# Performance work log

Hardware: AMD Instinct MI355X
Metric: run time of the kernel (lower is better)

Reference implementation:

```python
import jax, jax.numpy as jnp
import numpy as np

C = 0.1          # curvature
EPS = 1e-8
BN_EPS = 1e-5
MAX_NORM = 0.9

def batchnorm_train(x, gamma, beta):
    mu = jnp.mean(x, axis=0)
    var = jnp.var(x, axis=0)  # biased, matches torch BN normalization
    return gamma * (x - mu) * jax.lax.rsqrt(var + BN_EPS) + beta

def euclidean_to_poincare(x, c=C, max_norm=MAX_NORM):
    norm = jnp.linalg.norm(x, axis=-1, keepdims=True)
    zeros_mask = norm == 0
    safe_norm = jnp.where(zeros_mask, jnp.ones_like(norm), norm)
    sqrt_c = jnp.sqrt(jnp.asarray(c, x.dtype))
    scale = max_norm * jnp.tanh(sqrt_c * norm) / (sqrt_c * safe_norm)
    return jnp.where(zeros_mask, jnp.zeros_like(x), scale * x)

def poincare_to_euclidean(x, c=C):
    norms = jnp.linalg.norm(x, axis=-1, keepdims=True)
    norms = jnp.clip(norms, 1e-8, 1.0 - 1e-8)
    sqrt_c = jnp.sqrt(jnp.asarray(c, x.dtype))
    return x * jnp.arctanh(sqrt_c * norms) / (sqrt_c * norms)

def batch_poincare_exp_map(x, v, c=C):
    x_nsq = jnp.sum(x * x, axis=-1, keepdims=True)
    lambda_x = 2.0 / (1.0 - c * x_nsq + EPS)
    v_norm = jnp.linalg.norm(v, axis=-1, keepdims=True)
    v_norm = jnp.maximum(v_norm, EPS)
    sqrt_c = jnp.sqrt(jnp.asarray(c, x.dtype))
    scale = jnp.tanh(sqrt_c * lambda_x * v_norm / 2.0) / (sqrt_c * v_norm)
    sv = scale * v
    numerator = (1.0 - c * x_nsq) * sv
    x_sv = jnp.sum(x * sv, axis=-1, keepdims=True)
    sv_nsq = jnp.sum(sv * sv, axis=-1, keepdims=True)
    denom = 1.0 - 2.0 * c * x_sv + c * c * x_nsq * sv_nsq
    result = x + numerator / (denom + EPS)
    mask = jnp.all(jnp.isfinite(result), axis=-1, keepdims=True)
    return jnp.where(mask, result, jnp.zeros_like(result))

def batch_poincare_log_map(x, y, c=C):
    x_nsq = jnp.sum(x * x, axis=-1, keepdims=True)
    lambda_x = 2.0 / (1.0 - c * x_nsq + EPS)
    y_nsq = jnp.sum(y * y, axis=-1, keepdims=True)
    xy = jnp.sum(x * y, axis=-1, keepdims=True)
    numerator = (1.0 - 2.0 * c * xy + c * y_nsq) * x - (1.0 - c * x_nsq) * y
    denom = 1.0 - 2.0 * c * xy + c * c * x_nsq * y_nsq
    diff = numerator / (denom + EPS)
    diff_norm = jnp.linalg.norm(diff, axis=-1, keepdims=True)
    diff_norm = jnp.maximum(diff_norm, EPS)
    sqrt_c = jnp.sqrt(jnp.asarray(c, x.dtype))
    return 2.0 / (sqrt_c * lambda_x) * jnp.arctanh(sqrt_c * diff_norm) * diff / diff_norm

def setup_inputs() -> dict:
    key = jax.random.key(0)
    ks = jax.random.split(key, 8)
    B, D_IN, H, D_OUT = 8192, 1024, 2048, 1000
    x = jax.random.normal(ks[0], (B, D_IN), dtype=jnp.float32)
    # kaiming_normal fan_out: std = sqrt(2/fan_out) with fan_out = out_features
    W1 = jax.random.normal(ks[1], (H, D_IN), dtype=jnp.float32) * np.sqrt(2.0 / H)
    b1 = jnp.zeros((H,), jnp.float32)
    g1 = jnp.ones((H,), jnp.float32)
    be1 = jnp.zeros((H,), jnp.float32)
    W2 = jax.random.normal(ks[2], (H, H), dtype=jnp.float32) * np.sqrt(2.0 / H)
    b2 = jnp.zeros((H,), jnp.float32)
    g2 = jnp.ones((H,), jnp.float32)
    be2 = jnp.zeros((H,), jnp.float32)
    W3 = jax.random.normal(ks[3], (D_OUT, H), dtype=jnp.float32) * np.sqrt(2.0 / D_OUT)
    b3 = jnp.zeros((D_OUT,), jnp.float32)
    return {"x": x, "W1": W1, "b1": b1, "g1": g1, "be1": be1,
            "W2": W2, "b2": b2, "g2": g2, "be2": be2, "W3": W3, "b3": b3}

def reference(x, W1, b1, g1, be1, W2, b2, g2, be2, W3, b3):
    h1 = jax.nn.relu(batchnorm_train(x @ W1.T + b1, g1, be1))
    h1_hyp = euclidean_to_poincare(h1)
    origin = jnp.zeros_like(h1_hyp)
    h1_tan = batch_poincare_log_map(origin, h1_hyp)
    h2_tan = jax.nn.relu(batchnorm_train(h1_tan @ W2.T + b2, g2, be2))
    h2_hyp = batch_poincare_exp_map(origin, h2_tan)
    h2_euc = poincare_to_euclidean(h2_hyp)
    out = h2_euc @ W3.T + b3
    return jax.nn.log_softmax(out, axis=1)
```

## Files before the change

kernel.cpp:

```cpp
#include <hip/hip_runtime.h>

typedef __bf16 bf16x8 __attribute__((ext_vector_type(8)));
typedef float f32x16 __attribute__((ext_vector_type(16)));
typedef unsigned short us8 __attribute__((ext_vector_type(8)));

#define AS1 __attribute__((address_space(1)))
#define AS3 __attribute__((address_space(3)))

__device__ __forceinline__ unsigned short f2bf(float x) {
  unsigned int u = __float_as_uint(x);
  u += 0x7fffu + ((u >> 16) & 1u);
  return (unsigned short)(u >> 16);
}
__device__ __forceinline__ float bf2f(unsigned short u) {
  return __uint_as_float(((unsigned int)u) << 16);
}
__device__ __forceinline__ void async_copy16(const void* g, void* l) {
  __builtin_amdgcn_global_load_lds((AS1 void*)(g), (AS3 void*)(l), 16, 0, 0);
}

#define BARRIER() asm volatile("s_barrier" ::: "memory")
#define WAITV(n) asm volatile("s_waitcnt vmcnt(" #n ")" ::: "memory")

__global__ void __launch_bounds__(256) k_prep(const float* __restrict__ x,
                                              const float* __restrict__ W1,
                                              const float* __restrict__ W2,
                                              const float* __restrict__ W3,
                                              unsigned short* __restrict__ Xb,
                                              unsigned short* __restrict__ W1b,
                                              unsigned short* __restrict__ W2b,
                                              unsigned short* __restrict__ W3b,
                                              float* __restrict__ P) {
  const long n1 = 2097152, n2 = 524288, n3 = 1048576, n4 = 524288;
  long i = (long)blockIdx.x * 256 + threadIdx.x;
  const float* s = nullptr;
  unsigned short* d = nullptr;
  long j = i;
  if (i < n1)                { s = x;  d = Xb; }
  else if ((j -= n1) < n2)   { s = W1; d = W1b; }
  else if ((j -= n2) < n3)   { s = W2; d = W2b; }
  else if ((j -= n3) < n4) {
    ushort4 o;
    if ((j >> 9) < 1000) {
      float4 v = ((const float4*)W3)[j];
      o.x = f2bf(v.x); o.y = f2bf(v.y); o.z = f2bf(v.z); o.w = f2bf(v.w);
    } else { o.x = 0; o.y = 0; o.z = 0; o.w = 0; }
    ((ushort4*)W3b)[j] = o;
    return;
  } else {
    j -= n4;
    ((float4*)P)[j] = (float4){0.f, 0.f, 0.f, 0.f};
    return;
  }
  float4 v = ((const float4*)s)[j];
  ushort4 o;
  o.x = f2bf(v.x); o.y = f2bf(v.y); o.z = f2bf(v.z); o.w = f2bf(v.w);
  ((ushort4*)d)[j] = o;
}

template <bool OUTBF16, bool STATS>
__global__ void __launch_bounds__(512, 2) k_gemm(const unsigned short* __restrict__ A,
                                                 const unsigned short* __restrict__ B,
                                                 void* __restrict__ Cout,
                                                 void* __restrict__ Cout2, int K,
                                                 int lda, int ldb, int ldc,
                                                 float* __restrict__ P) {
  __shared__ __align__(16) unsigned short lA[2][256 * 64];
  __shared__ __align__(16) unsigned short lB[2][256 * 64];
  const int tid = threadIdx.x;
  const int wave = tid >> 6;
  const int lane = tid & 63;
  const int l31 = lane & 31;
  const int khi = lane >> 5;
  const int r7 = l31 & 7;
  const int wrh = wave >> 2;
  const int wcn = wave & 3;

  const int f = blockIdx.x + gridDim.x * blockIdx.y;
  const int xcd = f & 7;
  const int fi = f >> 3;
  const int nblk = fi % gridDim.x;
  const int mblk = fi / gridDim.x + (gridDim.y >> 3) * xcd;
  const long m0 = (long)mblk * 256;
  const long n0 = (long)nblk * 256;
  const long koff = (long)blockIdx.z * K;
  const int NT = K >> 6;

  const int rsub = lane >> 3;
  const int qg = ((lane & 7) ^ rsub) * 8;
  const unsigned short* gAq0 = A + (m0 +       8 * wave + rsub) * (long)lda + koff + qg;
  const unsigned short* gAq1 = A + (m0 +  64 + 8 * wave + rsub) * (long)lda + koff + qg;
  const unsigned short* gAq2 = A + (m0 + 128 + 8 * wave + rsub) * (long)lda + koff + qg;
  const unsigned short* gAq3 = A + (m0 + 192 + 8 * wave + rsub) * (long)lda + koff + qg;
  const unsigned short* gB0  = B + (n0 + 32 * wave + rsub) * (long)ldb + koff + qg;
  const unsigned short* gB1  = gB0 +  8 * (long)ldb;
  const unsigned short* gB2  = gB0 + 16 * (long)ldb;
  const unsigned short* gB3  = gB0 + 24 * (long)ldb;
  const int dAq0 = (      8 * wave) * 64;
  const int dAq1 = ( 64 + 8 * wave) * 64;
  const int dAq2 = (128 + 8 * wave) * 64;
  const int dAq3 = (192 + 8 * wave) * 64;
  const int dB0  = (32 * wave) * 64;

  f32x16 acc[4][2];
#pragma unroll
  for (int i = 0; i < 4; ++i)
#pragma unroll
    for (int j = 0; j < 2; ++j) acc[i][j] = (f32x16)(0.f);

#define PH_READS(rh, kh, DOB)                                                        \
  bf16x8 af[2][2];                                                                   \
  _Pragma("unroll") for (int i = 0; i < 2; ++i) {                                    \
    _Pragma("unroll") for (int ks = 0; ks < 2; ++ks) {                               \
      af[i][ks] = *(const bf16x8*)&lAc[(wrh * 128 + (rh) * 64 + i * 32 + l31) * 64 + \
                                       ((((kh) * 2 + ks) * 2 + khi) ^ r7) * 8];      \
    }                                                                                \
  }                                                                                  \
  if (DOB) {                                                                         \
    _Pragma("unroll") for (int j = 0; j < 2; ++j) {                                  \
      _Pragma("unroll") for (int ks = 0; ks < 2; ++ks) {                             \
        bf[j][ks] = *(const bf16x8*)&lBc[(wcn * 64 + j * 32 + l31) * 64 +            \
                                         ((((kh) * 2 + ks) * 2 + khi) ^ r7) * 8];    \
      }                                                                              \
    }                                                                                \
  }

#define PH_MFMA(rh)                                                                 \
  __builtin_amdgcn_s_setprio(1);                                                    \
  _Pragma("unroll") for (int ks = 0; ks < 2; ++ks) {                                 \
    _Pragma("unroll") for (int i = 0; i < 2; ++i) {                                  \
      _Pragma("unroll") for (int j = 0; j < 2; ++j) {                                \
        acc[(rh) * 2 + i][j] = __builtin_amdgcn_mfma_f32_32x32x16_bf16(              \
            af[i][ks], bf[j][ks], acc[(rh) * 2 + i][j], 0, 0, 0);                    \
      }                                                                              \
    }                                                                                \
  }                                                                                  \
  __builtin_amdgcn_s_setprio(0);

  {
    unsigned short* lAn = &lA[0][0];
    unsigned short* lBn = &lB[0][0];
    async_copy16(gAq0, lAn + dAq0);
    async_copy16(gAq2, lAn + dAq2);
    async_copy16(gB0,  lBn + dB0);
    async_copy16(gB1,  lBn + dB0 + 8 * 64);
    async_copy16(gB2,  lBn + dB0 + 16 * 64);
    async_copy16(gB3,  lBn + dB0 + 24 * 64);
    async_copy16(gAq1, lAn + dAq1);
    async_copy16(gAq3, lAn + dAq3);
    WAITV(2);
    BARRIER();
  }

  for (int t = 0; t < NT - 1; ++t) {
    const unsigned short* lAc = &lA[t & 1][0];
    const unsigned short* lBc = &lB[t & 1][0];
    unsigned short* lAn = &lA[(t + 1) & 1][0];
    unsigned short* lBn = &lB[(t + 1) & 1][0];
    const long kk = (long)(t + 1) * 64;
    bf16x8 bf[2][2];
    {
      PH_READS(0, 0, 1)
      async_copy16(gAq0 + kk, lAn + dAq0);
      async_copy16(gAq2 + kk, lAn + dAq2);
      BARRIER();
      PH_MFMA(0)
      WAITV(2);
      BARRIER();
    }
    {
      PH_READS(1, 0, 0)
      async_copy16(gB0 + kk, lBn + dB0);
      async_copy16(gB1 + kk, lBn + dB0 + 8 * 64);
      BARRIER();
      PH_MFMA(1)
      BARRIER();
    }
    {
      PH_READS(0, 1, 1)
      async_copy16(gB2 + kk, lBn + dB0 + 16 * 64);
      async_copy16(gB3 + kk, lBn + dB0 + 24 * 64);
      BARRIER();
      PH_MFMA(0)
      BARRIER();
    }
    {
      PH_READS(1, 1, 0)
      async_copy16(gAq1 + kk, lAn + dAq1);
      async_copy16(gAq3 + kk, lAn + dAq3);
      BARRIER();
      PH_MFMA(1)
      WAITV(2);
      BARRIER();
    }
  }

  {
    const unsigned short* lAc = &lA[(NT - 1) & 1][0];
    const unsigned short* lBc = &lB[(NT - 1) & 1][0];
    bf16x8 bf[2][2];
    { PH_READS(0, 0, 1) BARRIER(); PH_MFMA(0) WAITV(0); BARRIER(); }
    { PH_READS(1, 0, 0) BARRIER(); PH_MFMA(1) BARRIER(); }
    { PH_READS(0, 1, 1) BARRIER(); PH_MFMA(0) BARRIER(); }
    { PH_READS(1, 1, 0) BARRIER(); PH_MFMA(1) BARRIER(); }
  }
#undef PH_READS
#undef PH_MFMA

  const int rbase = 4 * khi;
  const long crow0 = m0 + wrh * 128;
  const long ccol0 = n0 + wcn * 64;
  if (OUTBF16) {
    unsigned short* C = (unsigned short*)(blockIdx.z ? Cout2 : Cout);
#pragma unroll
    for (int ig = 0; ig < 4; ++ig)
#pragma unroll
      for (int j = 0; j < 2; ++j) {
        long col = ccol0 + j * 32 + l31;
#pragma unroll
        for (int reg = 0; reg < 16; ++reg) {
          long row = crow0 + ig * 32 + (reg & 3) + 8 * (reg >> 2) + rbase;
          C[row * (long)ldc + col] = f2bf(acc[ig][j][reg]);
        }
      }
  } else {
    float* C = (float*)(blockIdx.z ? Cout2 : Cout);
#pragma unroll
    for (int ig = 0; ig < 4; ++ig)
#pragma unroll
      for (int j = 0; j < 2; ++j) {
        long col = ccol0 + j * 32 + l31;
#pragma unroll
        for (int reg = 0; reg < 16; ++reg) {
          long row = crow0 + ig * 32 + (reg & 3) + 8 * (reg >> 2) + rbase;
          C[row * (long)ldc + col] = acc[ig][j][reg];
        }
      }
  }

  if (STATS) {
    float* sred = (float*)&lA[0][0];
    sred[tid] = 0.f;
    __syncthreads();
#pragma unroll
    for (int j = 0; j < 2; ++j) {
      float s = 0.f, s2 = 0.f;
#pragma unroll
      for (int ig = 0; ig < 4; ++ig)
#pragma unroll
        for (int reg = 0; reg < 16; ++reg) {
          float v = acc[ig][j][reg];
          s += v;
          s2 = fmaf(v, v, s2);
        }
      int cl = wcn * 64 + j * 32 + l31;
      atomicAdd(&sred[cl], s);
      atomicAdd(&sred[256 + cl], s2);
    }
    __syncthreads();
    if (tid < 256) atomicAdd(&P[n0 + tid], sred[tid]);
    else           atomicAdd(&P[2048 + n0 + tid - 256], sred[tid]);
  }
}

__global__ void __launch_bounds__(256) k_bnfin(float* __restrict__ P,
                                               const float* __restrict__ g,
                                               const float* __restrict__ be) {
  const int c = blockIdx.x * 256 + threadIdx.x;
  float mean = P[c] * (1.f / 8192.f);
  float var = P[2048 + c] * (1.f / 8192.f) - mean * mean;
  float a = g[c] * rsqrtf(var + 1e-5f);
  P[c] = a;
  P[2048 + c] = be[c] - mean * a;
}

template <bool STAGE2>
__global__ void __launch_bounds__(256) k_fuse(const unsigned short* __restrict__ Zb,
                                              const float* __restrict__ P,
                                              unsigned short* __restrict__ Ab) {
  const int t = threadIdx.x, wave = t >> 6, lane = t & 63;
  const long row = (long)blockIdx.x * 4 + wave;

  float sc[32], sh[32];
#pragma unroll
  for (int c = 0; c < 4; ++c) {
    int b4 = (lane + 64 * c) * 2;
    float4 a0 = ((const float4*)P)[b4],       a1 = ((const float4*)P)[b4 + 1];
    float4 h0 = ((const float4*)P)[512 + b4], h1 = ((const float4*)P)[512 + b4 + 1];
    sc[c * 8 + 0] = a0.x; sc[c * 8 + 1] = a0.y; sc[c * 8 + 2] = a0.z; sc[c * 8 + 3] = a0.w;
    sc[c * 8 + 4] = a1.x; sc[c * 8 + 5] = a1.y; sc[c * 8 + 6] = a1.z; sc[c * 8 + 7] = a1.w;
    sh[c * 8 + 0] = h0.x; sh[c * 8 + 1] = h0.y; sh[c * 8 + 2] = h0.z; sh[c * 8 + 3] = h0.w;
    sh[c * 8 + 4] = h1.x; sh[c * 8 + 5] = h1.y; sh[c * 8 + 6] = h1.z; sh[c * 8 + 7] = h1.w;
  }

  const us8* zr = (const us8*)(Zb + row * 2048);
  float v[32];
  float ss = 0.f;
#pragma unroll
  for (int c = 0; c < 4; ++c) {
    us8 z8 = zr[lane + 64 * c];
#pragma unroll
    for (int j = 0; j < 8; ++j) {
      float xv = fmaxf(fmaf(bf2f(z8[j]), sc[c * 8 + j], sh[c * 8 + j]), 0.f);
      v[c * 8 + j] = xv;
      ss = fmaf(xv, xv, ss);
    }
  }
#pragma unroll
  for (int o = 32; o > 0; o >>= 1) ss += __shfl_xor(ss, o, 64);
  float n2 = ss;

  const float rsc = 0.31622776601683794f;
  float fac;
  if (STAGE2) {
    float nn = sqrtf(n2);
    float vn = fmaxf(nn, 1e-8f);
    float tt = rsc * vn;
    float scl = tanhf(tt) / tt;
    float hn = scl * nn;
    float cn = fminf(fmaxf(hn, 1e-8f), 1.0f);
    float z = rsc * cn;
    fac = scl * (atanhf(z) / z);
  } else {
    fac = 0.f;
    if (n2 > 0.f) {
      float n = sqrtf(n2);
      float th = tanhf(rsc * n);
      float s = 0.9f * th / (rsc * n);
      float dn = fmaxf(s * n, 1e-8f);
      float z = rsc * dn;
      fac = -(atanhf(z) / z) * s;
    }
  }
  us8* dr = (us8*)(Ab + row * 2048);
#pragma unroll
  for (int c = 0; c < 4; ++c) {
    us8 o8;
#pragma unroll
    for (int j = 0; j < 8; ++j) o8[j] = f2bf(v[c * 8 + j] * fac);
    dr[lane + 64 * c] = o8;
  }
}

__global__ void __launch_bounds__(256) k_lsm(const unsigned short* __restrict__ Za,
                                             const unsigned short* __restrict__ Zb2,
                                             const float* __restrict__ b3,
                                             float* __restrict__ out) {
  const int t = threadIdx.x, wave = t >> 6, lane = t & 63;
  const long row = (long)blockIdx.x * 4 + wave;
  const us8* za8 = (const us8*)(Za + row * 1024);
  const us8* zb8 = (const us8*)(Zb2 + row * 1024);

  float v[16];
  float mx = -3.4e38f;
#pragma unroll
  for (int c = 0; c < 2; ++c) {
    const bool ok = (c == 0) | (lane < 61);
    if (ok) {
      us8 a8 = za8[c * 64 + lane];
      us8 b8 = zb8[c * 64 + lane];
      const float* bp = b3 + c * 512 + lane * 8;
      float4 bA = *(const float4*)bp;
      float4 bB = *(const float4*)(bp + 4);
      float bb[8] = {bA.x, bA.y, bA.z, bA.w, bB.x, bB.y, bB.z, bB.w};
#pragma unroll
      for (int j = 0; j < 8; ++j) {
        float x = bf2f(a8[j]) + bf2f(b8[j]) + bb[j];
        v[c * 8 + j] = x;
        mx = fmaxf(mx, x);
      }
    } else {
#pragma unroll
      for (int j = 0; j < 8; ++j) v[c * 8 + j] = -3.4e38f;
    }
  }
#pragma unroll
  for (int o = 32; o > 0; o >>= 1) mx = fmaxf(mx, __shfl_xor(mx, o, 64));

  float se = 0.f;
#pragma unroll
  for (int c = 0; c < 2; ++c)
#pragma unroll
    for (int j = 0; j < 8; ++j)
      if ((c == 0) | (lane < 61)) se += expf(v[c * 8 + j] - mx);
#pragma unroll
  for (int o = 32; o > 0; o >>= 1) se += __shfl_xor(se, o, 64);
  float mls = mx + logf(se);

  float* orow = out + row * 1000;
#pragma unroll
  for (int c = 0; c < 2; ++c) {
    if ((c == 0) | (lane < 61)) {
      float4 o0 = {v[c * 8 + 0] - mls, v[c * 8 + 1] - mls, v[c * 8 + 2] - mls, v[c * 8 + 3] - mls};
      float4 o1 = {v[c * 8 + 4] - mls, v[c * 8 + 5] - mls, v[c * 8 + 6] - mls, v[c * 8 + 7] - mls};
      float* op = orow + c * 512 + lane * 8;
      *(float4*)op = o0;
      *(float4*)(op + 4) = o1;
    }
  }
}

extern "C" void kernel_launch(void* const* d_in, const int* in_sizes, int n_in,
                              void* d_out, int out_size, void* d_ws, size_t ws_size,
                              hipStream_t stream) {
  (void)in_sizes; (void)n_in; (void)out_size; (void)ws_size;
  const float* x   = (const float*)d_in[0];
  const float* W1  = (const float*)d_in[1];
  const float* g1  = (const float*)d_in[3];
  const float* be1 = (const float*)d_in[4];
  const float* W2  = (const float*)d_in[5];
  const float* g2  = (const float*)d_in[7];
  const float* be2 = (const float*)d_in[8];
  const float* W3  = (const float*)d_in[9];
  const float* b3  = (const float*)d_in[10];
  float* out = (float*)d_out;

  char* ws = (char*)d_ws;
  size_t off = 0;
  auto alloc = [&](size_t bytes) {
    void* p = ws + off;
    off += (bytes + 255) & ~(size_t)255;
    return p;
  };
  unsigned short* Xb  = (unsigned short*)alloc((size_t)8192 * 1024 * 2);
  unsigned short* W1b = (unsigned short*)alloc((size_t)2048 * 1024 * 2);
  unsigned short* W2b = (unsigned short*)alloc((size_t)2048 * 2048 * 2);
  unsigned short* W3b = (unsigned short*)alloc((size_t)1024 * 2048 * 2);
  unsigned short* Zb  = (unsigned short*)alloc((size_t)8192 * 2048 * 2);
  unsigned short* Ab  = (unsigned short*)alloc((size_t)8192 * 2048 * 2);
  unsigned short* Z3a = (unsigned short*)alloc((size_t)8192 * 1024 * 2);
  float* P            = (float*)alloc((size_t)2 * 4096 * 4);
  float* P2 = P + 4096;
  unsigned short* Z3b = Zb;

  k_prep<<<16392, 256, 0, stream>>>(x, W1, W2, W3, Xb, W1b, W2b, W3b, P);

  k_gemm<true, true><<<dim3(8, 32, 1), 512, 0, stream>>>(Xb, W1b, Zb, Zb, 1024, 1024, 1024, 2048, P);
  k_bnfin<<<8, 256, 0, stream>>>(P, g1, be1);
  k_fuse<false><<<2048, 256, 0, stream>>>(Zb, P, Ab);

  k_gemm<true, true><<<dim3(8, 32, 1), 512, 0, stream>>>(Ab, W2b, Zb, Zb, 2048, 2048, 2048, 2048, P2);
  k_bnfin<<<8, 256, 0, stream>>>(P2, g2, be2);
  k_fuse<true><<<2048, 256, 0, stream>>>(Zb, P2, Ab);

  k_gemm<true, false><<<dim3(4, 32, 2), 512, 0, stream>>>(Ab, W3b, Z3a, Z3b, 1024, 2048, 2048, 1024, nullptr);
  k_lsm<<<2048, 256, 0, stream>>>(Z3a, Z3b, b3, out);
}
```

Measured before the change: 298.3 us.

## Fuse all stages into one persistent kernel with grid-wide atomic barriers

Replaces the chain of nine launches (prep, three GEMMs, two BN finalizes, two fuse kernels, log-softmax) with one persistent 256-block kernel. Stages are separated by software grid barriers built on atomic counters. The BN finalize step is folded into each block's fuse stage through shared memory. The aim is to remove launch gaps and tail effects between kernels, at the cost of spin-wait barriers. It also relies on all 256 blocks being co-resident, and conversion and elementwise stages now run with only 256 blocks.

After: 453.5 us. +52.0%, slower.

```diff
diff --git a/kernel.cpp b/kernel.cpp
--- a/kernel.cpp
+++ b/kernel.cpp
@@ -22,51 +22,25 @@
 #define BARRIER() asm volatile("s_barrier" ::: "memory")
 #define WAITV(n) asm volatile("s_waitcnt vmcnt(" #n ")" ::: "memory")
 
-__global__ void __launch_bounds__(256) k_prep(const float* __restrict__ x,
-                                              const float* __restrict__ W1,
-                                              const float* __restrict__ W2,
-                                              const float* __restrict__ W3,
-                                              unsigned short* __restrict__ Xb,
-                                              unsigned short* __restrict__ W1b,
-                                              unsigned short* __restrict__ W2b,
-                                              unsigned short* __restrict__ W3b,
-                                              float* __restrict__ P) {
-  const long n1 = 2097152, n2 = 524288, n3 = 1048576, n4 = 524288;
-  long i = (long)blockIdx.x * 256 + threadIdx.x;
-  const float* s = nullptr;
-  unsigned short* d = nullptr;
-  long j = i;
-  if (i < n1)                { s = x;  d = Xb; }
-  else if ((j -= n1) < n2)   { s = W1; d = W1b; }
-  else if ((j -= n2) < n3)   { s = W2; d = W2b; }
-  else if ((j -= n3) < n4) {
-    ushort4 o;
-    if ((j >> 9) < 1000) {
-      float4 v = ((const float4*)W3)[j];
-      o.x = f2bf(v.x); o.y = f2bf(v.y); o.z = f2bf(v.z); o.w = f2bf(v.w);
-    } else { o.x = 0; o.y = 0; o.z = 0; o.w = 0; }
-    ((ushort4*)W3b)[j] = o;
-    return;
-  } else {
-    j -= n4;
-    ((float4*)P)[j] = (float4){0.f, 0.f, 0.f, 0.f};
-    return;
-  }
-  float4 v = ((const float4*)s)[j];
-  ushort4 o;
-  o.x = f2bf(v.x); o.y = f2bf(v.y); o.z = f2bf(v.z); o.w = f2bf(v.w);
-  ((ushort4*)d)[j] = o;
-}
-
-template <bool OUTBF16, bool STATS>
-__global__ void __launch_bounds__(512, 2) k_gemm(const unsigned short* __restrict__ A,
-                                                 const unsigned short* __restrict__ B,
-                                                 void* __restrict__ Cout,
-                                                 void* __restrict__ Cout2, int K,
-                                                 int lda, int ldb, int ldc,
-                                                 float* __restrict__ P) {
-  __shared__ __align__(16) unsigned short lA[2][256 * 64];
-  __shared__ __align__(16) unsigned short lB[2][256 * 64];
+__device__ __forceinline__ void gsync(unsigned* bar, int slot) {
+  __syncthreads();
+  if (threadIdx.x == 0) {
+    __hip_atomic_fetch_add(&bar[slot], 1u, __ATOMIC_RELEASE, __HIP_MEMORY_SCOPE_AGENT);
+    while (__hip_atomic_load(&bar[slot], __ATOMIC_ACQUIRE, __HIP_MEMORY_SCOPE_AGENT) < 256u)
+      __builtin_amdgcn_s_sleep(2);
+    __threadfence();
+  }
+  __syncthreads();
+}
+
+template <bool STATS>
+__device__ __forceinline__ void gemm_body(int f, int NBX, int NBY,
+                                          const unsigned short* __restrict__ A,
+                                          const unsigned short* __restrict__ B,
+                                          unsigned short* __restrict__ C, int K,
+                                          int lda, int ldb, int ldc, long koff,
+                                          float* __restrict__ P,
+                                          unsigned short* lAb, unsigned short* lBb) {
   const int tid = threadIdx.x;
   const int wave = tid >> 6;
   const int lane = tid & 63;
@@ -76,14 +50,12 @@
   const int wrh = wave >> 2;
   const int wcn = wave & 3;
 
-  const int f = blockIdx.x + gridDim.x * blockIdx.y;
   const int xcd = f & 7;
   const int fi = f >> 3;
-  const int nblk = fi % gridDim.x;
-  const int mblk = fi / gridDim.x + (gridDim.y >> 3) * xcd;
+  const int nblk = fi % NBX;
+  const int mblk = fi / NBX + (NBY >> 3) * xcd;
   const long m0 = (long)mblk * 256;
   const long n0 = (long)nblk * 256;
-  const long koff = (long)blockIdx.z * K;
   const int NT = K >> 6;
 
   const int rsub = lane >> 3;
@@ -138,8 +110,8 @@
   __builtin_amdgcn_s_setprio(0);
 
   {
-    unsigned short* lAn = &lA[0][0];
-    unsigned short* lBn = &lB[0][0];
+    unsigned short* lAn = lAb;
+    unsigned short* lBn = lBb;
     async_copy16(gAq0, lAn + dAq0);
     async_copy16(gAq2, lAn + dAq2);
     async_copy16(gB0,  lBn + dB0);
@@ -153,10 +125,10 @@
   }
 
   for (int t = 0; t < NT - 1; ++t) {
-    const unsigned short* lAc = &lA[t & 1][0];
-    const unsigned short* lBc = &lB[t & 1][0];
-    unsigned short* lAn = &lA[(t + 1) & 1][0];
-    unsigned short* lBn = &lB[(t + 1) & 1][0];
+    const unsigned short* lAc = lAb + (t & 1) * 16384;
+    const unsigned short* lBc = lBb + (t & 1) * 16384;
+    unsigned short* lAn = lAb + ((t + 1) & 1) * 16384;
+    unsigned short* lBn = lBb + ((t + 1) & 1) * 16384;
     const long kk = (long)(t + 1) * 64;
     bf16x8 bf[2][2];
     {
@@ -196,8 +168,8 @@
   }
 
   {
-    const unsigned short* lAc = &lA[(NT - 1) & 1][0];
-    const unsigned short* lBc = &lB[(NT - 1) & 1][0];
+    const unsigned short* lAc = lAb + ((NT - 1) & 1) * 16384;
+    const unsigned short* lBc = lBb + ((NT - 1) & 1) * 16384;
     bf16x8 bf[2][2];
     { PH_READS(0, 0, 1) BARRIER(); PH_MFMA(0) WAITV(0); BARRIER(); }
     { PH_READS(1, 0, 0) BARRIER(); PH_MFMA(1) BARRIER(); }
@@ -210,36 +182,20 @@
   const int rbase = 4 * khi;
   const long crow0 = m0 + wrh * 128;
   const long ccol0 = n0 + wcn * 64;
-  if (OUTBF16) {
-    unsigned short* C = (unsigned short*)(blockIdx.z ? Cout2 : Cout);
-#pragma unroll
-    for (int ig = 0; ig < 4; ++ig)
-#pragma unroll
-      for (int j = 0; j < 2; ++j) {
-        long col = ccol0 + j * 32 + l31;
-#pragma unroll
-        for (int reg = 0; reg < 16; ++reg) {
-          long row = crow0 + ig * 32 + (reg & 3) + 8 * (reg >> 2) + rbase;
-          C[row * (long)ldc + col] = f2bf(acc[ig][j][reg]);
-        }
-      }
-  } else {
-    float* C = (float*)(blockIdx.z ? Cout2 : Cout);
-#pragma unroll
-    for (int ig = 0; ig < 4; ++ig)
-#pragma unroll
-      for (int j = 0; j < 2; ++j) {
-        long col = ccol0 + j * 32 + l31;
-#pragma unroll
-        for (int reg = 0; reg < 16; ++reg) {
-          long row = crow0 + ig * 32 + (reg & 3) + 8 * (reg >> 2) + rbase;
-          C[row * (long)ldc + col] = acc[ig][j][reg];
-        }
-      }
-  }
+#pragma unroll
+  for (int ig = 0; ig < 4; ++ig)
+#pragma unroll
+    for (int j = 0; j < 2; ++j) {
+      long col = ccol0 + j * 32 + l31;
+#pragma unroll
+      for (int reg = 0; reg < 16; ++reg) {
+        long row = crow0 + ig * 32 + (reg & 3) + 8 * (reg >> 2) + rbase;
+        C[row * (long)ldc + col] = f2bf(acc[ig][j][reg]);
+      }
+    }
 
   if (STATS) {
-    float* sred = (float*)&lA[0][0];
+    float* sred = (float*)lAb;
     sred[tid] = 0.f;
     __syncthreads();
 #pragma unroll
@@ -263,141 +219,228 @@
   }
 }
 
-__global__ void __launch_bounds__(256) k_bnfin(float* __restrict__ P,
-                                               const float* __restrict__ g,
-                                               const float* __restrict__ be) {
-  const int c = blockIdx.x * 256 + threadIdx.x;
-  float mean = P[c] * (1.f / 8192.f);
-  float var = P[2048 + c] * (1.f / 8192.f) - mean * mean;
-  float a = g[c] * rsqrtf(var + 1e-5f);
-  P[c] = a;
-  P[2048 + c] = be[c] - mean * a;
-}
-
 template <bool STAGE2>
-__global__ void __launch_bounds__(256) k_fuse(const unsigned short* __restrict__ Zb,
-                                              const float* __restrict__ P,
-                                              unsigned short* __restrict__ Ab) {
-  const int t = threadIdx.x, wave = t >> 6, lane = t & 63;
-  const long row = (long)blockIdx.x * 4 + wave;
+__device__ __forceinline__ void bnfuse_body(int b, const float* __restrict__ P,
+                                            const float* __restrict__ g,
+                                            const float* __restrict__ be,
+                                            const unsigned short* __restrict__ Zb,
+                                            unsigned short* __restrict__ Ab,
+                                            float* scsh) {
+  const int tid = threadIdx.x, wave = tid >> 6, lane = tid & 63;
+  {
+    float4 s = ((const float4*)P)[tid];
+    float4 q = ((const float4*)P)[512 + tid];
+    float4 gg = ((const float4*)g)[tid];
+    float4 bb = ((const float4*)be)[tid];
+    float sm[4] = {s.x, s.y, s.z, s.w}, sq[4] = {q.x, q.y, q.z, q.w};
+    float gv[4] = {gg.x, gg.y, gg.z, gg.w}, bv[4] = {bb.x, bb.y, bb.z, bb.w};
+#pragma unroll
+    for (int k = 0; k < 4; ++k) {
+      float mean = sm[k] * (1.f / 8192.f);
+      float var = sq[k] * (1.f / 8192.f) - mean * mean;
+      float a = gv[k] * rsqrtf(var + 1e-5f);
+      scsh[tid * 4 + k] = a;
+      scsh[2048 + tid * 4 + k] = bv[k] - mean * a;
+    }
+  }
+  __syncthreads();
 
   float sc[32], sh[32];
 #pragma unroll
   for (int c = 0; c < 4; ++c) {
-    int b4 = (lane + 64 * c) * 2;
-    float4 a0 = ((const float4*)P)[b4],       a1 = ((const float4*)P)[b4 + 1];
-    float4 h0 = ((const float4*)P)[512 + b4], h1 = ((const float4*)P)[512 + b4 + 1];
+    int cb = (lane + 64 * c) * 8;
+    float4 a0 = *(const float4*)&scsh[cb],        a1 = *(const float4*)&scsh[cb + 4];
+    float4 h0 = *(const float4*)&scsh[2048 + cb], h1 = *(const float4*)&scsh[2048 + cb + 4];
     sc[c * 8 + 0] = a0.x; sc[c * 8 + 1] = a0.y; sc[c * 8 + 2] = a0.z; sc[c * 8 + 3] = a0.w;
     sc[c * 8 + 4] = a1.x; sc[c * 8 + 5] = a1.y; sc[c * 8 + 6] = a1.z; sc[c * 8 + 7] = a1.w;
     sh[c * 8 + 0] = h0.x; sh[c * 8 + 1] = h0.y; sh[c * 8 + 2] = h0.z; sh[c * 8 + 3] = h0.w;
     sh[c * 8 + 4] = h1.x; sh[c * 8 + 5] = h1.y; sh[c * 8 + 6] = h1.z; sh[c * 8 + 7] = h1.w;
   }
 
-  const us8* zr = (const us8*)(Zb + row * 2048);
-  float v[32];
-  float ss = 0.f;
-#pragma unroll
-  for (int c = 0; c < 4; ++c) {
-    us8 z8 = zr[lane + 64 * c];
-#pragma unroll
-    for (int j = 0; j < 8; ++j) {
-      float xv = fmaxf(fmaf(bf2f(z8[j]), sc[c * 8 + j], sh[c * 8 + j]), 0.f);
-      v[c * 8 + j] = xv;
-      ss = fmaf(xv, xv, ss);
-    }
-  }
-#pragma unroll
-  for (int o = 32; o > 0; o >>= 1) ss += __shfl_xor(ss, o, 64);
-  float n2 = ss;
-
   const float rsc = 0.31622776601683794f;
-  float fac;
-  if (STAGE2) {
-    float nn = sqrtf(n2);
-    float vn = fmaxf(nn, 1e-8f);
-    float tt = rsc * vn;
-    float scl = tanhf(tt) / tt;
-    float hn = scl * nn;
-    float cn = fminf(fmaxf(hn, 1e-8f), 1.0f);
-    float z = rsc * cn;
-    fac = scl * (atanhf(z) / z);
-  } else {
-    fac = 0.f;
-    if (n2 > 0.f) {
-      float n = sqrtf(n2);
-      float th = tanhf(rsc * n);
-      float s = 0.9f * th / (rsc * n);
-      float dn = fmaxf(s * n, 1e-8f);
-      float z = rsc * dn;
-      fac = -(atanhf(z) / z) * s;
-    }
-  }
-  us8* dr = (us8*)(Ab + row * 2048);
-#pragma unroll
-  for (int c = 0; c < 4; ++c) {
-    us8 o8;
-#pragma unroll
-    for (int j = 0; j < 8; ++j) o8[j] = f2bf(v[c * 8 + j] * fac);
-    dr[lane + 64 * c] = o8;
-  }
-}
-
-__global__ void __launch_bounds__(256) k_lsm(const unsigned short* __restrict__ Za,
-                                             const unsigned short* __restrict__ Zb2,
-                                             const float* __restrict__ b3,
-                                             float* __restrict__ out) {
-  const int t = threadIdx.x, wave = t >> 6, lane = t & 63;
-  const long row = (long)blockIdx.x * 4 + wave;
-  const us8* za8 = (const us8*)(Za + row * 1024);
-  const us8* zb8 = (const us8*)(Zb2 + row * 1024);
-
-  float v[16];
-  float mx = -3.4e38f;
-#pragma unroll
-  for (int c = 0; c < 2; ++c) {
-    const bool ok = (c == 0) | (lane < 61);
-    if (ok) {
-      us8 a8 = za8[c * 64 + lane];
-      us8 b8 = zb8[c * 64 + lane];
-      const float* bp = b3 + c * 512 + lane * 8;
-      float4 bA = *(const float4*)bp;
-      float4 bB = *(const float4*)(bp + 4);
-      float bb[8] = {bA.x, bA.y, bA.z, bA.w, bB.x, bB.y, bB.z, bB.w};
+#pragma unroll 1
+  for (int r = 0; r < 4; ++r) {
+    const long row = (long)b * 32 + r * 8 + wave;
+    const us8* zr = (const us8*)(Zb + row * 2048);
+    float v[32];
+    float ss = 0.f;
+#pragma unroll
+    for (int c = 0; c < 4; ++c) {
+      us8 z8 = zr[lane + 64 * c];
 #pragma unroll
       for (int j = 0; j < 8; ++j) {
-        float x = bf2f(a8[j]) + bf2f(b8[j]) + bb[j];
-        v[c * 8 + j] = x;
-        mx = fmaxf(mx, x);
-      }
+        float xv = fmaxf(fmaf(bf2f(z8[j]), sc[c * 8 + j], sh[c * 8 + j]), 0.f);
+        v[c * 8 + j] = xv;
+        ss = fmaf(xv, xv, ss);
+      }
+    }
+#pragma unroll
+    for (int o = 32; o > 0; o >>= 1) ss += __shfl_xor(ss, o, 64);
+    float n2 = ss;
+
+    float fac;
+    if (STAGE2) {
+      float nn = sqrtf(n2);
+      float vn = fmaxf(nn, 1e-8f);
+      float tt = rsc * vn;
+      float scl = tanhf(tt) / tt;
+      float hn = scl * nn;
+      float cn = fminf(fmaxf(hn, 1e-8f), 1.0f);
+      float z = rsc * cn;
+      fac = scl * (atanhf(z) / z);
     } else {
-#pragma unroll
-      for (int j = 0; j < 8; ++j) v[c * 8 + j] = -3.4e38f;
-    }
-  }
-#pragma unroll
-  for (int o = 32; o > 0; o >>= 1) mx = fmaxf(mx, __shfl_xor(mx, o, 64));
-
-  float se = 0.f;
-#pragma unroll
-  for (int c = 0; c < 2; ++c)
-#pragma unroll
-    for (int j = 0; j < 8; ++j)
-      if ((c == 0) | (lane < 61)) se += expf(v[c * 8 + j] - mx);
-#pragma unroll
-  for (int o = 32; o > 0; o >>= 1) se += __shfl_xor(se, o, 64);
-  float mls = mx + logf(se);
-
-  float* orow = out + row * 1000;
-#pragma unroll
-  for (int c = 0; c < 2; ++c) {
-    if ((c == 0) | (lane < 61)) {
-      float4 o0 = {v[c * 8 + 0] - mls, v[c * 8 + 1] - mls, v[c * 8 + 2] - mls, v[c * 8 + 3] - mls};
-      float4 o1 = {v[c * 8 + 4] - mls, v[c * 8 + 5] - mls, v[c * 8 + 6] - mls, v[c * 8 + 7] - mls};
-      float* op = orow + c * 512 + lane * 8;
-      *(float4*)op = o0;
-      *(float4*)(op + 4) = o1;
-    }
-  }
+      fac = 0.f;
+      if (n2 > 0.f) {
+        float n = sqrtf(n2);
+        float th = tanhf(rsc * n);
+        float s = 0.9f * th / (rsc * n);
+        float dn = fmaxf(s * n, 1e-8f);
+        float z = rsc * dn;
+        fac = -(atanhf(z) / z) * s;
+      }
+    }
+    us8* dr = (us8*)(Ab + row * 2048);
+#pragma unroll
+    for (int c = 0; c < 4; ++c) {
+      us8 o8;
+#pragma unroll
+      for (int j = 0; j < 8; ++j) o8[j] = f2bf(v[c * 8 + j] * fac);
+      dr[lane + 64 * c] = o8;
+    }
+  }
+}
+
+__device__ __forceinline__ void lsm_body(int b, const unsigned short* __restrict__ Za,
+                                         const unsigned short* __restrict__ Zb2,
+                                         const float* __restrict__ b3,
+                                         float* __restrict__ out) {
+  const int tid = threadIdx.x, wave = tid >> 6, lane = tid & 63;
+#pragma unroll 1
+  for (int r = 0; r < 4; ++r) {
+    const long row = (long)b * 32 + r * 8 + wave;
+    const us8* za8 = (const us8*)(Za + row * 1024);
+    const us8* zb8 = (const us8*)(Zb2 + row * 1024);
+
+    float v[16];
+    float mx = -3.4e38f;
+#pragma unroll
+    for (int c = 0; c < 2; ++c) {
+      const bool ok = (c == 0) | (lane < 61);
+      if (ok) {
+        us8 a8 = za8[c * 64 + lane];
+        us8 b8 = zb8[c * 64 + lane];
+        const float* bp = b3 + c * 512 + lane * 8;
+        float4 bA = *(const float4*)bp;
+        float4 bB = *(const float4*)(bp + 4);
+        float bb[8] = {bA.x, bA.y, bA.z, bA.w, bB.x, bB.y, bB.z, bB.w};
+#pragma unroll
+        for (int j = 0; j < 8; ++j) {
+          float x = bf2f(a8[j]) + bf2f(b8[j]) + bb[j];
+          v[c * 8 + j] = x;
+          mx = fmaxf(mx, x);
+        }
+      } else {
+#pragma unroll
+        for (int j = 0; j < 8; ++j) v[c * 8 + j] = -3.4e38f;
+      }
+    }
+#pragma unroll
+    for (int o = 32; o > 0; o >>= 1) mx = fmaxf(mx, __shfl_xor(mx, o, 64));
+
+    float se = 0.f;
+#pragma unroll
+    for (int c = 0; c < 2; ++c)
+#pragma unroll
+      for (int j = 0; j < 8; ++j)
+        if ((c == 0) | (lane < 61)) se += expf(v[c * 8 + j] - mx);
+#pragma unroll
+    for (int o = 32; o > 0; o >>= 1) se += __shfl_xor(se, o, 64);
+    float mls = mx + logf(se);
+
+    float* orow = out + row * 1000;
+#pragma unroll
+    for (int c = 0; c < 2; ++c) {
+      if ((c == 0) | (lane < 61)) {
+        float4 o0 = {v[c * 8 + 0] - mls, v[c * 8 + 1] - mls, v[c * 8 + 2] - mls, v[c * 8 + 3] - mls};
+        float4 o1 = {v[c * 8 + 4] - mls, v[c * 8 + 5] - mls, v[c * 8 + 6] - mls, v[c * 8 + 7] - mls};
+        float* op = orow + c * 512 + lane * 8;
+        *(float4*)op = o0;
+        *(float4*)(op + 4) = o1;
+      }
+    }
+  }
+}
+
+__global__ void __launch_bounds__(512, 2) k_mega(
+    const float* __restrict__ x, const float* __restrict__ W1,
+    const float* __restrict__ g1, const float* __restrict__ be1,
+    const float* __restrict__ W2, const float* __restrict__ g2,
+    const float* __restrict__ be2, const float* __restrict__ W3,
+    const float* __restrict__ b3,
+    unsigned short* __restrict__ Xb, unsigned short* __restrict__ W1b,
+    unsigned short* __restrict__ W2b, unsigned short* __restrict__ W3b,
+    unsigned short* __restrict__ Zb, unsigned short* __restrict__ Ab,
+    unsigned short* __restrict__ Z3a, float* __restrict__ P1,
+    float* __restrict__ P2, unsigned* __restrict__ bar,
+    float* __restrict__ out) {
+  __shared__ __align__(16) unsigned short lA[2][256 * 64];
+  __shared__ __align__(16) unsigned short lB[2][256 * 64];
+  const int b = blockIdx.x;
+  const int tid = threadIdx.x;
+  unsigned short* Z3b = Zb;
+
+  {
+    const long n1 = 2097152, n2 = 524288, n3 = 1048576;
+    long i = (long)b * 512 + tid;
+#pragma unroll 1
+    for (int it = 0; it < 32; ++it, i += 131072) {
+      long j = i;
+      const float* s;
+      unsigned short* d;
+      if (i < n1)              { s = x;  d = Xb; }
+      else if ((j -= n1) < n2) { s = W1; d = W1b; }
+      else if ((j -= n2) < n3) { s = W2; d = W2b; }
+      else {
+        j -= n3;
+        ushort4 o;
+        if ((j >> 9) < 1000) {
+          float4 v = ((const float4*)W3)[j];
+          o.x = f2bf(v.x); o.y = f2bf(v.y); o.z = f2bf(v.z); o.w = f2bf(v.w);
+        } else { o.x = 0; o.y = 0; o.z = 0; o.w = 0; }
+        ((ushort4*)W3b)[j] = o;
+        continue;
+      }
+      float4 v = ((const float4*)s)[j];
+      ushort4 o;
+      o.x = f2bf(v.x); o.y = f2bf(v.y); o.z = f2bf(v.z); o.w = f2bf(v.w);
+      ((ushort4*)d)[j] = o;
+    }
+  }
+  gsync(bar, 0);
+
+  gemm_body<true>(b, 8, 32, Xb, W1b, Zb, 1024, 1024, 1024, 2048, 0, P1,
+                  &lA[0][0], &lB[0][0]);
+  gsync(bar, 1);
+
+  bnfuse_body<false>(b, P1, g1, be1, Zb, Ab, (float*)&lA[0][0]);
+  gsync(bar, 2);
+
+  gemm_body<true>(b, 8, 32, Ab, W2b, Zb, 2048, 2048, 2048, 2048, 0, P2,
+                  &lA[0][0], &lB[0][0]);
+  gsync(bar, 3);
+
+  bnfuse_body<true>(b, P2, g2, be2, Zb, Ab, (float*)&lA[0][0]);
+  gsync(bar, 4);
+
+  {
+    const int z = b >> 7;
+    const int f = b & 127;
+    gemm_body<false>(f, 4, 32, Ab, W3b, z ? Z3b : Z3a, 1024, 2048, 2048, 1024,
+                     (long)z * 1024, nullptr, &lA[0][0], &lB[0][0]);
+  }
+  gsync(bar, 5);
+
+  lsm_body(b, Z3a, Z3b, b3, out);
 }
 
 extern "C" void kernel_launch(void* const* d_in, const int* in_sizes, int n_in,
@@ -429,20 +472,13 @@
   unsigned short* Zb  = (unsigned short*)alloc((size_t)8192 * 2048 * 2);
   unsigned short* Ab  = (unsigned short*)alloc((size_t)8192 * 2048 * 2);
   unsigned short* Z3a = (unsigned short*)alloc((size_t)8192 * 1024 * 2);
-  float* P            = (float*)alloc((size_t)2 * 4096 * 4);
+  float* P            = (float*)alloc((size_t)2 * 4096 * 4 + 256);
   float* P2 = P + 4096;
-  unsigned short* Z3b = Zb;
-
-  k_prep<<<16392, 256, 0, stream>>>(x, W1, W2, W3, Xb, W1b, W2b, W3b, P);
-
-  k_gemm<true, true><<<dim3(8, 32, 1), 512, 0, stream>>>(Xb, W1b, Zb, Zb, 1024, 1024, 1024, 2048, P);
-  k_bnfin<<<8, 256, 0, stream>>>(P, g1, be1);
-  k_fuse<false><<<2048, 256, 0, stream>>>(Zb, P, Ab);
-
-  k_gemm<true, true><<<dim3(8, 32, 1), 512, 0, stream>>>(Ab, W2b, Zb, Zb, 2048, 2048, 2048, 2048, P2);
-  k_bnfin<<<8, 256, 0, stream>>>(P2, g2, be2);
-  k_fuse<true><<<2048, 256, 0, stream>>>(Zb, P2, Ab);
-
-  k_gemm<true, false><<<dim3(4, 32, 2), 512, 0, stream>>>(Ab, W3b, Z3a, Z3b, 1024, 2048, 2048, 1024, nullptr);
-  k_lsm<<<2048, 256, 0, stream>>>(Z3a, Z3b, b3, out);
-}
+  unsigned* bar = (unsigned*)(P + 8192);
+
+  hipMemsetAsync(P, 0, (size_t)2 * 4096 * 4 + 256, stream);
+
+  k_mega<<<256, 512, 0, stream>>>(x, W1, g1, be1, W2, g2, be2, W3, b3,
+                                  Xb, W1b, W2b, W3b, Zb, Ab, Z3a,
+                                  P, P2, bar, out);
+}
```
